# Performance work log

Hardware: AMD Instinct MI355X
Metric: run time of the kernel (lower is better)

Reference implementation:

```python
import jax, jax.numpy as jnp
import numpy as np

N_DRUG, N_DIS = 100_000, 50_000
E1, E2 = 500_000, 250_000
D, H = 128, 4
HD = D // H          # 32
EAD, CONT, CARD = 32, 4, 8


def _segment_softmax(logits, seg, num_segments):
    # logits: [E, H], seg: [E] -> softmax normalized per destination node (PyG softmax)
    m = jax.ops.segment_max(logits, seg, num_segments=num_segments)
    m = jnp.where(jnp.isfinite(m), m, 0.0)  # empty segments
    ex = jnp.exp(logits - m[seg])
    s = jax.ops.segment_sum(ex, seg, num_segments=num_segments)
    return ex / (s[seg] + 1e-16)


def _edge_conv(src_x, dst_x, si, di, Wsrc, bsrc, Wdst, bdst, attn, gate):
    num_dst = dst_x.shape[0]
    msg_src = src_x[si] @ Wsrc + bsrc            # [E, D]
    msg_dst = dst_x[di] @ Wdst + bdst            # [E, D]
    msg = msg_src + msg_dst
    if gate is not None:
        msg = msg * gate
    E = msg.shape[0]
    mh = msg.reshape(E, H, HD)
    sh = msg_src.reshape(E, H, HD)
    dh = msg_dst.reshape(E, H, HD)
    logits = (sh * dh).sum(-1) * (1.0 / np.sqrt(HD)) + (mh * attn[None]).sum(-1)  # [E, H]
    w = _segment_softmax(logits, di, num_dst)    # [E, H]; dropout p applied only in training
    out = (mh * w[..., None]).reshape(E, D)
    return jax.ops.segment_sum(out, di, num_segments=num_dst)  # [num_dst, D]


def setup_inputs() -> dict:
    key = jax.random.key(0)
    it = iter(jax.random.split(key, 32))
    def nrm(shape, s=0.05):
        return jax.random.normal(next(it), shape, jnp.float32) * s
    def ri(hi, shape):
        return jax.random.randint(next(it), shape, 0, hi, jnp.int32)
    z = lambda n: jnp.zeros((n,), jnp.float32)
    return {
        "x_drug": nrm((N_DRUG, D), 1.0),
        "x_dis": nrm((N_DIS, D), 1.0),
        "e1_cont": nrm((E1, CONT), 1.0),
        "W_src1": nrm((D, D)), "b_src1": z(D),
        "W_dst1": nrm((D, D)), "b_dst1": z(D),
        "attn1": nrm((H, HD)),
        "emb1": nrm((CARD, EAD)),
        "gW1": nrm((EAD + CONT, D)), "gb1": z(D),
        "gW2": nrm((D, D)), "gb2": z(D),
        "W_src2": nrm((D, D)), "b_src2": z(D),
        "W_dst2": nrm((D, D)), "b_dst2": z(D),
        "attn2": nrm((H, HD)),
        "Wo_drug": nrm((D, D)), "bo_drug": z(D),
        "Wo_dis": nrm((D, D)), "bo_dis": z(D),
        "e1_src": ri(N_DRUG, (E1,)), "e1_dst": ri(N_DRUG, (E1,)),
        "e2_src": ri(N_DRUG, (E2,)), "e2_dst": ri(N_DIS, (E2,)),
        "e1_cat": ri(CARD, (E1,)),
    }


def reference(x_drug, x_dis, e1_cont, W_src1, b_src1, W_dst1, b_dst1, attn1,
              emb1, gW1, gb1, gW2, gb2, W_src2, b_src2, W_dst2, b_dst2, attn2,
              Wo_drug, bo_drug, Wo_dis, bo_dis,
              e1_src, e1_dst, e2_src, e2_dst, e1_cat):
    # drug -> drug edges, spec mixed (1 categorical + 4 continuous): gated messages
    gate_feat = jnp.concatenate([emb1[e1_cat], e1_cont], axis=-1)  # [E1, EAD+CONT]
    gate = jax.nn.sigmoid(
        jax.nn.gelu(gate_feat @ gW1 + gb1, approximate=False) @ gW2 + gb2)  # [E1, D]
    aggr_drug = _edge_conv(x_drug, x_drug, e1_src, e1_dst,
                           W_src1, b_src1, W_dst1, b_dst1, attn1, gate)
    # drug -> disease edges, spec none: no gate
    aggr_dis = _edge_conv(x_drug, x_dis, e2_src, e2_dst,
                          W_src2, b_src2, W_dst2, b_dst2, attn2, None)
    # one message list per dst node type -> mean over a single element == identity
    out_drug = aggr_drug @ Wo_drug + bo_drug
    out_dis = aggr_dis @ Wo_dis + bo_dis
    return (out_drug, out_dis)
```

## Files before the change

kernel.cpp:

```cpp
#include <hip/hip_runtime.h>
#include <hip/hip_bf16.h>
#include <math.h>

#define ND 100000
#define NS 50000
#define NE1 500000
#define NE2 250000
#define DIM 128
#define NH 4
#define HDI 32
#define GRID_M 512
#define GRID_G 1024
#define GRID_E1 2048
#define GRID_E2 1024
#define NT1 (NE1 / 16)
#define NT2 (NE2 / 16)

typedef __hip_bfloat16 bf16;
typedef unsigned short u16;
typedef unsigned int u32;
typedef short sx8 __attribute__((ext_vector_type(8)));
typedef float fx4 __attribute__((ext_vector_type(4)));

__device__ __forceinline__ float ldf(const float* p, size_t i) { return p[i]; }
__device__ __forceinline__ float ldf(const bf16* p, size_t i) { return __bfloat162float(p[i]); }
__device__ __forceinline__ float b2f(bf16 v) { return __bfloat162float(v); }

__device__ __forceinline__ u16 f2bfu(float f) {
    __hip_bfloat16 h = __float2bfloat16(f);
    union { __hip_bfloat16 b; u16 u; } c; c.b = h; return c.u;
}
__device__ __forceinline__ float2 bfp(u32 u) {
    float2 r;
    r.x = __uint_as_float(u << 16);
    r.y = __uint_as_float(u & 0xffff0000u);
    return r;
}
__device__ __forceinline__ sx8 pack8(float4 v0, float4 v1) {
    sx8 r;
    r[0] = (short)f2bfu(v0.x); r[1] = (short)f2bfu(v0.y);
    r[2] = (short)f2bfu(v0.z); r[3] = (short)f2bfu(v0.w);
    r[4] = (short)f2bfu(v1.x); r[5] = (short)f2bfu(v1.y);
    r[6] = (short)f2bfu(v1.z); r[7] = (short)f2bfu(v1.w);
    return r;
}
__device__ __forceinline__ sx8 lda8(const bf16* p) { return *(const sx8*)p; }
__device__ __forceinline__ sx8 lda8(const float* p) {
    return pack8(*(const float4*)p, *(const float4*)(p + 4));
}
__device__ __forceinline__ float4 ld4(const float* p) { return *(const float4*)p; }
__device__ __forceinline__ float4 ld4(const bf16* p) {
    float2 a = bfp(*(const u32*)p);
    float2 b = bfp(*(const u32*)(p + 2));
    return make_float4(a.x, a.y, b.x, b.y);
}

__device__ __forceinline__ float gelu_fast(float x) {
    float u2 = x * fmaf(x * x, 0.0713550f, 1.5957691f);
    u2 = fminf(u2, 40.0f);
    float t = __expf(u2);
    return x * t * __builtin_amdgcn_rcpf(t + 1.0f);
}
__device__ __forceinline__ float sigmoid_fast(float x) {
    return __builtin_amdgcn_rcpf(1.0f + __expf(-x));
}
__device__ __forceinline__ float exp_fast(float x) { return __expf(x); }

__device__ __forceinline__ void slab_store(float* Gw, const fx4* acc, int er, int lg) {
#pragma unroll
    for (int f = 0; f < 8; ++f)
#pragma unroll
        for (int r = 0; r < 4; ++r) {
            int row = 4 * lg + r;
            int byo = row * 512 + (((16 * f + er) * 4) ^ ((row & 7) << 4));
            *(float*)((char*)Gw + byo) = acc[f][r];
        }
}
__device__ __forceinline__ void slab_flush_bf16(const float* Gw, int lane, bf16* Yrow) {
#pragma unroll
    for (int i = 0; i < 16; ++i) {
        float2 gv = *(const float2*)((const char*)Gw + i * 512 + ((lane * 8) ^ ((i & 7) << 4)));
        u32 pk = ((u32)f2bfu(gv.y) << 16) | (u32)f2bfu(gv.x);
        *(u32*)&Yrow[(size_t)i * DIM + 2 * lane] = pk;
    }
}
__device__ __forceinline__ void sty2(float* p, float2 v) { *(float2*)p = v; }
__device__ __forceinline__ void sty2(bf16* p, float2 v) {
    *(u32*)p = ((u32)f2bfu(v.y) << 16) | (u32)f2bfu(v.x);
}

__global__ void fill16_kernel(u16* p, u16 v, size_t n) {
    size_t i = (size_t)blockIdx.x * blockDim.x + threadIdx.x;
    if (i < n) p[i] = v;
}

__global__ __launch_bounds__(64) void detect_kernel(const u16* w, int* flag) {
    int lane = threadIdx.x;
    int mx = 0;
    for (int j = 0; j < 32; ++j) {
        int i = 2 * (lane + 64 * j);
        int e = (w[i] >> 7) & 0xFF;
        mx = mx > e ? mx : e;
    }
    for (int d = 32; d; d >>= 1) { int o = __shfl_xor(mx, d); mx = mx > o ? mx : o; }
    if (lane == 0) flag[0] = (mx >= 0x90) ? 1 : 0;
}

__global__ __launch_bounds__(256) void hist_kernel(const int* __restrict__ dst, int ne,
                                                   u32* __restrict__ cnt) {
    int stride = gridDim.x * blockDim.x;
    for (int i = blockIdx.x * blockDim.x + threadIdx.x; i < ne; i += stride)
        atomicAdd(&cnt[dst[i]], 1u);
}

__global__ __launch_bounds__(256) void scanA_kernel(const u32* __restrict__ cnt, int nb,
                                                    u32* __restrict__ chk) {
    __shared__ u32 ws[4];
    int b = blockIdx.x, t = threadIdx.x;
    int i0 = b * 1024 + t * 4;
    u32 s = 0;
#pragma unroll
    for (int j = 0; j < 4; ++j) { int i = i0 + j; if (i < nb) s += cnt[i]; }
#pragma unroll
    for (int d = 1; d < 64; d <<= 1) s += __shfl_xor(s, d);
    if ((t & 63) == 0) ws[t >> 6] = s;
    __syncthreads();
    if (t == 0) chk[b] = ws[0] + ws[1] + ws[2] + ws[3];
}

__global__ __launch_bounds__(256) void scanB_kernel(u32* __restrict__ chk, int nc) {
    __shared__ u32 sh[256];
    int t = threadIdx.x;
    u32 v = (t < nc) ? chk[t] : 0u;
    sh[t] = v;
    __syncthreads();
    for (int d = 1; d < 256; d <<= 1) {
        u32 x = (t >= d) ? sh[t - d] : 0u;
        __syncthreads();
        if (t >= d) sh[t] += x;
        __syncthreads();
    }
    if (t < nc) chk[t] = sh[t] - v;
}

__global__ __launch_bounds__(256) void scanC_kernel(const u32* __restrict__ cnt, int nb,
                                                    const u32* __restrict__ chk,
                                                    u32* __restrict__ offs) {
    __shared__ u32 wsum[4];
    int b = blockIdx.x, t = threadIdx.x, lane = t & 63, wv = t >> 6;
    int i0 = b * 1024 + t * 4;
    u32 c0 = (i0 + 0 < nb) ? cnt[i0 + 0] : 0u;
    u32 c1 = (i0 + 1 < nb) ? cnt[i0 + 1] : 0u;
    u32 c2 = (i0 + 2 < nb) ? cnt[i0 + 2] : 0u;
    u32 c3 = (i0 + 3 < nb) ? cnt[i0 + 3] : 0u;
    u32 tot = c0 + c1 + c2 + c3;
    u32 inc = tot;
#pragma unroll
    for (int d = 1; d < 64; d <<= 1) { u32 x = __shfl_up(inc, d); if (lane >= d) inc += x; }
    if (lane == 63) wsum[wv] = inc;
    __syncthreads();
    u32 base = chk[b] + (inc - tot);
    for (int k = 0; k < wv; ++k) base += wsum[k];
    if (i0 + 0 < nb) offs[i0 + 0] = base;
    if (i0 + 1 < nb) offs[i0 + 1] = base + c0;
    if (i0 + 2 < nb) offs[i0 + 2] = base + c0 + c1;
    if (i0 + 3 < nb) offs[i0 + 3] = base + c0 + c1 + c2;
}

__global__ __launch_bounds__(256) void scatter_kernel(const int* __restrict__ dst, int ne,
                                                      u32* __restrict__ offs,
                                                      u32* __restrict__ perm) {
    int stride = gridDim.x * blockDim.x;
    for (int i = blockIdx.x * blockDim.x + threadIdx.x; i < ne; i += stride) {
        u32 p = atomicAdd(&offs[dst[i]], 1u);
        perm[p] = (u32)i;
    }
}

template <typename T>
__device__ __forceinline__ void transp(const T* W, u16* Bt, int gtid, int gstride) {
    for (int i = gtid; i < DIM * DIM; i += gstride) {
        int n = i >> 7, k = i & 127;
        Bt[i] = f2bfu(ldf(W, (size_t)k * DIM + n));
    }
}

template <typename T>
__device__ __forceinline__ void prep_body(
    const T* emb, const T* gW1, const T* gb1, const T* gW2,
    const T* Ws1, const T* Wd1, const T* Ws2, const T* Wd2, const T* Wod, const T* Wos,
    u16* B1t, float* gb2f, const T* gb2,
    u16* Btg, u16* Bs1, u16* Bd1, u16* Bs2, u16* Bd2, u16* Bod, u16* Bos)
{
    int gtid = blockIdx.x * blockDim.x + threadIdx.x;
    int gstride = gridDim.x * blockDim.x;
    for (int i = gtid; i < DIM * 32; i += gstride) {
        int n = i >> 5, k = i & 31;
        float v = 0.0f;
        if (k < 8) {
            v = ldf(gb1, n);
            for (int q = 0; q < 32; ++q) v += ldf(emb, k * 32 + q) * ldf(gW1, (size_t)q * DIM + n);
        } else if (k < 12) {
            v = ldf(gW1, (size_t)(32 + (k - 8)) * DIM + n);
        }
        B1t[i] = f2bfu(v);
    }
    for (int i = gtid; i < DIM; i += gstride) gb2f[i] = ldf(gb2, i);
    transp(gW2, Btg, gtid, gstride);
    transp(Ws1, Bs1, gtid, gstride);
    transp(Wd1, Bd1, gtid, gstride);
    transp(Ws2, Bs2, gtid, gstride);
    transp(Wd2, Bd2, gtid, gstride);
    transp(Wod, Bod, gtid, gstride);
    transp(Wos, Bos, gtid, gstride);
}

__global__ __launch_bounds__(256) void prep_kernel(
    const int* __restrict__ flag,
    const void* emb, const void* gW1, const void* gb1, const void* gW2, const void* gb2,
    const void* Ws1, const void* Wd1, const void* Ws2, const void* Wd2,
    const void* Wod, const void* Wos,
    u16* __restrict__ B1t, float* __restrict__ gb2f,
    u16* __restrict__ Btg, u16* __restrict__ Bs1, u16* __restrict__ Bd1,
    u16* __restrict__ Bs2, u16* __restrict__ Bd2, u16* __restrict__ Bod,
    u16* __restrict__ Bos)
{
    if (flag[0])
        prep_body((const float*)emb, (const float*)gW1, (const float*)gb1, (const float*)gW2,
                  (const float*)Ws1, (const float*)Wd1, (const float*)Ws2, (const float*)Wd2,
                  (const float*)Wod, (const float*)Wos,
                  B1t, gb2f, (const float*)gb2, Btg, Bs1, Bd1, Bs2, Bd2, Bod, Bos);
    else
        prep_body((const bf16*)emb, (const bf16*)gW1, (const bf16*)gb1, (const bf16*)gW2,
                  (const bf16*)Ws1, (const bf16*)Wd1, (const bf16*)Ws2, (const bf16*)Wd2,
                  (const bf16*)Wod, (const bf16*)Wos,
                  B1t, gb2f, (const bf16*)gb2, Btg, Bs1, Bd1, Bs2, Bd2, Bod, Bos);
}

template <typename T>
__device__ __forceinline__ void proj2m_body(
    float* Gw, const T* X, const T* b1, const T* b2,
    const u16* Bt1, const u16* Bt2, bf16* Y1, bf16* Y2, int N)
{
    int tid = threadIdx.x, lane = tid & 63, er = lane & 15, lg = lane >> 4;
    float c1i[8], c2i[8];
#pragma unroll
    for (int f = 0; f < 8; ++f) {
        c1i[f] = ldf(b1, 16 * f + er);
        c2i[f] = ldf(b2, 16 * f + er);
    }
    const int NW = GRID_M * 4;
    int gwid = blockIdx.x * 4 + (tid >> 6);
    int tiles = N / 16;
    for (int t = gwid; t < tiles; t += NW) {
        const T* xr = X + (size_t)(t * 16 + er) * DIM;
        sx8 a[4];
#pragma unroll
        for (int ks = 0; ks < 4; ++ks) a[ks] = lda8(xr + ks * 32 + lg * 8);
        fx4 acc1[8], acc2[8];
#pragma unroll
        for (int f = 0; f < 8; ++f) {
            acc1[f][0] = c1i[f]; acc1[f][1] = c1i[f]; acc1[f][2] = c1i[f]; acc1[f][3] = c1i[f];
            acc2[f][0] = c2i[f]; acc2[f][1] = c2i[f]; acc2[f][2] = c2i[f]; acc2[f][3] = c2i[f];
        }
#pragma unroll
        for (int ks = 0; ks < 4; ++ks)
#pragma unroll
            for (int f = 0; f < 8; ++f) {
                sx8 bv1 = *(const sx8*)(Bt1 + (size_t)(16 * f + er) * DIM + ks * 32 + lg * 8);
                acc1[f] = __builtin_amdgcn_mfma_f32_16x16x32_bf16(a[ks], bv1, acc1[f], 0, 0, 0);
                sx8 bv2 = *(const sx8*)(Bt2 + (size_t)(16 * f + er) * DIM + ks * 32 + lg * 8);
                acc2[f] = __builtin_amdgcn_mfma_f32_16x16x32_bf16(a[ks], bv2, acc2[f], 0, 0, 0);
            }
        slab_store(Gw, acc1, er, lg);
        slab_flush_bf16(Gw, lane, Y1 + (size_t)t * 16 * DIM);
        slab_store(Gw, acc2, er, lg);
        slab_flush_bf16(Gw, lane, Y2 + (size_t)t * 16 * DIM);
    }
}

__global__ __launch_bounds__(256) void proj2m_kernel(
    const int* __restrict__ flag, const void* X, const void* b1, const void* b2,
    const u16* __restrict__ Bt1, const u16* __restrict__ Bt2,
    bf16* __restrict__ Y1, bf16* __restrict__ Y2, int N)
{
    __shared__ float Gt[4][16 * 128];
    float* Gw = Gt[threadIdx.x >> 6];
    if (flag[0]) proj2m_body(Gw, (const float*)X, (const float*)b1, (const float*)b2, Bt1, Bt2, Y1, Y2, N);
    else         proj2m_body(Gw, (const bf16*)X, (const bf16*)b1, (const bf16*)b2, Bt1, Bt2, Y1, Y2, N);
}

template <typename T>
__device__ __forceinline__ void proj1m_body(
    float* Gw, const T* X, const T* b, const u16* Bt, bf16* Y, int N)
{
    int tid = threadIdx.x, lane = tid & 63, er = lane & 15, lg = lane >> 4;
    float ci[8];
#pragma unroll
    for (int f = 0; f < 8; ++f) ci[f] = ldf(b, 16 * f + er);
    const int NW = GRID_M * 4;
    int gwid = blockIdx.x * 4 + (tid >> 6);
    int tiles = N / 16;
    for (int t = gwid; t < tiles; t += NW) {
        const T* xr = X + (size_t)(t * 16 + er) * DIM;
        sx8 a[4];
#pragma unroll
        for (int ks = 0; ks < 4; ++ks) a[ks] = lda8(xr + ks * 32 + lg * 8);
        fx4 acc[8];
#pragma unroll
        for (int f = 0; f < 8; ++f) {
            acc[f][0] = ci[f]; acc[f][1] = ci[f]; acc[f][2] = ci[f]; acc[f][3] = ci[f];
        }
#pragma unroll
        for (int ks = 0; ks < 4; ++ks)
#pragma unroll
            for (int f = 0; f < 8; ++f) {
                sx8 bv = *(const sx8*)(Bt + (size_t)(16 * f + er) * DIM + ks * 32 + lg * 8);
                acc[f] = __builtin_amdgcn_mfma_f32_16x16x32_bf16(a[ks], bv, acc[f], 0, 0, 0);
            }
        slab_store(Gw, acc, er, lg);
        slab_flush_bf16(Gw, lane, Y + (size_t)t * 16 * DIM);
    }
}

__global__ __launch_bounds__(256) void proj1m_kernel(
    const int* __restrict__ flag, const void* X, const void* b,
    const u16* __restrict__ Bt, bf16* __restrict__ Y, int N)
{
    __shared__ float Gt[4][16 * 128];
    float* Gw = Gt[threadIdx.x >> 6];
    if (flag[0]) proj1m_body(Gw, (const float*)X, (const float*)b, Bt, Y, N);
    else         proj1m_body(Gw, (const bf16*)X, (const bf16*)b, Bt, Y, N);
}

template <typename T>
__device__ __forceinline__ void projoutm_body(
    float* Gw, const float* A, const float* s, const T* b,
    const u16* Bt, T* out, int N)
{
    int tid = threadIdx.x, lane = tid & 63, er = lane & 15, lg = lane >> 4;
    float ci[8];
#pragma unroll
    for (int f = 0; f < 8; ++f) ci[f] = ldf(b, 16 * f + er);
    const int NW = GRID_M * 4;
    int gwid = blockIdx.x * 4 + (tid >> 6);
    int tiles = N / 16;
    for (int t = gwid; t < tiles; t += NW) {
        const float* ar = A + (size_t)(t * 16 + er) * DIM;
        const float* sr = s + (size_t)(t * 16 + er) * NH;
        sx8 a[4];
#pragma unroll
        for (int ks = 0; ks < 4; ++ks) {
            float inv = 1.0f / (sr[ks] + 1e-16f);
            float4 v0 = *(const float4*)(ar + ks * 32 + lg * 8);
            float4 v1 = *(const float4*)(ar + ks * 32 + lg * 8 + 4);
            v0.x *= inv; v0.y *= inv; v0.z *= inv; v0.w *= inv;
            v1.x *= inv; v1.y *= inv; v1.z *= inv; v1.w *= inv;
            a[ks] = pack8(v0, v1);
        }
        fx4 acc[8];
#pragma unroll
        for (int f = 0; f < 8; ++f) {
            acc[f][0] = ci[f]; acc[f][1] = ci[f]; acc[f][2] = ci[f]; acc[f][3] = ci[f];
        }
#pragma unroll
        for (int ks = 0; ks < 4; ++ks)
#pragma unroll
            for (int f = 0; f < 8; ++f) {
                sx8 bv = *(const sx8*)(Bt + (size_t)(16 * f + er) * DIM + ks * 32 + lg * 8);
                acc[f] = __builtin_amdgcn_mfma_f32_16x16x32_bf16(a[ks], bv, acc[f], 0, 0, 0);
            }
        slab_store(Gw, acc, er, lg);
#pragma unroll
        for (int i = 0; i < 16; ++i) {
            float2 gv = *(const float2*)((const char*)Gw + i * 512 + ((lane * 8) ^ ((i & 7) << 4)));
            sty2(out + (size_t)(t * 16 + i) * DIM + 2 * lane, gv);
        }
    }
}

__global__ __launch_bounds__(256) void projoutm_kernel(
    const int* __restrict__ flag, const float* __restrict__ A, const float* __restrict__ s,
    const void* b, const u16* __restrict__ Bt, void* out, size_t off, int N)
{
    __shared__ float Gt[4][16 * 128];
    float* Gw = Gt[threadIdx.x >> 6];
    if (flag[0]) projoutm_body(Gw, A, s, (const float*)b, Bt, (float*)out + off, N);
    else         projoutm_body(Gw, A, s, (const bf16*)b, Bt, (bf16*)out + off, N);
}

template <typename T>
__device__ __forceinline__ void gateall_body(
    float* Gw, const int* cat, const T* econt,
    const float* gb2f, const u16* B1t, const u16* Btg,
    const u32* perm, u32* gates, int c0, int c1)
{
    int tid = threadIdx.x;
    int lane = tid & 63;
    int er = lane & 15, lg = lane >> 4;

    float cinit[8];
#pragma unroll
    for (int f = 0; f < 8; ++f) cinit[f] = gb2f[16 * f + er];

    const int NW = GRID_G * 4;
    int span = c1 - c0;
    int w = blockIdx.x * 4 + (tid >> 6);
    int tpw = (span + NW - 1) / NW;
    int t0 = c0 + w * tpw, t1 = t0 + tpw;
    if (t1 > c1) t1 = c1;

    const fx4 zf = {0.f, 0.f, 0.f, 0.f};

    int c = 0;
    float4 fv = make_float4(0.f, 0.f, 0.f, 0.f);
    if (t0 < t1) {
        int e = (int)perm[t0 * 16 + er];
        c = cat[e];
        fv = ld4(econt + (size_t)e * 4);
    }

    for (int t = t0; t < t1; ++t) {
        int tn = t + 1;
        int e_n = (tn < t1) ? (int)perm[tn * 16 + er] : 0;
        int c_n = cat[e_n];
        float4 fv_n = ld4(econt + (size_t)e_n * 4);

        sx8 a1;
#pragma unroll
        for (int j = 0; j < 8; ++j) a1[j] = 0;
        if (lg == 0) {
#pragma unroll
            for (int j = 0; j < 8; ++j) a1[j] = (c == j) ? (short)0x3F80 : (short)0;
        } else if (lg == 1) {
            a1[0] = (short)f2bfu(fv.x); a1[1] = (short)f2bfu(fv.y);
            a1[2] = (short)f2bfu(fv.z); a1[3] = (short)f2bfu(fv.w);
        }

        fx4 p1[8];
#pragma unroll
        for (int f = 0; f < 8; ++f) {
            sx8 b1 = *(const sx8*)(B1t + (size_t)(16 * f + er) * 32 + lg * 8);
            p1[f] = __builtin_amdgcn_mfma_f32_16x16x32_bf16(a1, b1, zf, 0, 0, 0);
        }

#pragma unroll
        for (int f = 0; f < 8; ++f)
#pragma unroll
            for (int r = 0; r < 4; ++r) {
                int row = 4 * lg + r;
                float hg = gelu_fast(p1[f][r]);
                int byo = row * 512 + (((16 * f + er) * 4) ^ ((row & 7) << 4));
                *(float*)((char*)Gw + byo) = hg;
            }

        sx8 a2[4];
#pragma unroll
        for (int ks = 0; ks < 4; ++ks) {
            int base = ks * 128 + lg * 32;
            float4 v0 = *(const float4*)((const char*)Gw + er * 512 + ((base)      ^ ((er & 7) << 4)));
            float4 v1 = *(const float4*)((const char*)Gw + er * 512 + ((base + 16) ^ ((er & 7) << 4)));
            a2[ks] = pack8(v0, v1);
        }

        fx4 acc[8];
#pragma unroll
        for (int f = 0; f < 8; ++f) {
            acc[f][0] = cinit[f]; acc[f][1] = cinit[f];
            acc[f][2] = cinit[f]; acc[f][3] = cinit[f];
        }
#pragma unroll
        for (int ks = 0; ks < 4; ++ks) {
#pragma unroll
            for (int f = 0; f < 8; ++f) {
                sx8 b = *(const sx8*)(Btg + (size_t)(16 * f + er) * DIM + ks * 32 + lg * 8);
                acc[f] = __builtin_amdgcn_mfma_f32_16x16x32_bf16(a2[ks], b, acc[f], 0, 0, 0);
            }
        }

#pragma unroll
        for (int f = 0; f < 8; ++f)
#pragma unroll
            for (int r = 0; r < 4; ++r) {
                int row = 4 * lg + r;
                float g = sigmoid_fast(acc[f][r]);
                int byo = row * 512 + (((16 * f + er) * 4) ^ ((row & 7) << 4));
                *(float*)((char*)Gw + byo) = g;
            }

#pragma unroll
        for (int i = 0; i < 16; ++i) {
            float2 gv = *(const float2*)((const char*)Gw + i * 512 + ((lane * 8) ^ ((i & 7) << 4)));
            u32 pk = ((u32)f2bfu(gv.y) << 16) | (u32)f2bfu(gv.x);
            gates[((size_t)(t - c0) * 16 + i) * 64 + lane] = pk;
        }

        c = c_n; fv = fv_n;
    }
}

__global__ __launch_bounds__(256) void gateall_kernel(
    const int* __restrict__ flag, const int* __restrict__ cat, const void* econt,
    const float* __restrict__ gb2f, const u16* __restrict__ B1t,
    const u16* __restrict__ Btg,
    const u32* __restrict__ perm, u32* __restrict__ gates, int c0, int c1)
{
    __shared__ float Gt[4][16 * 128];
    float* Gw = Gt[threadIdx.x >> 6];
    if (flag[0]) gateall_body(Gw, cat, (const float*)econt, gb2f, B1t, Btg, perm, gates, c0, c1);
    else         gateall_body(Gw, cat, (const bf16*)econt, gb2f, B1t, Btg, perm, gates, c0, c1);
}

template <typename T>
__device__ __forceinline__ void edge1e_body(
    const bf16* Xs, const bf16* Xd,
    const int* src, const int* dst,
    const T* attn, const u32* perm, const u32* gates, int c0, int c1,
    float* s_out, float* aggr)
{
    int tid = threadIdx.x;
    int lane = tid & 63;
    int d0 = 2 * lane, h = lane >> 4, k0 = d0 & 31;
    float av0 = ldf(attn, h * HDI + k0), av1 = ldf(attn, h * HDI + k0 + 1);
    const float rs = 0.17677669529663688110f;

    const int NW = GRID_E1 * 4;
    int span = c1 - c0;
    int w = blockIdx.x * 4 + (tid >> 6);
    int cpw = (span + NW - 1) / NW;
    int t0 = c0 + w * cpw, t1 = t0 + cpw;
    if (t1 > c1) t1 = c1;

    int cur_di = -1;
    float acc0 = 0.f, acc1 = 0.f, ssum = 0.f;

    u32 sv = 0, dv = 0;
    if (t0 < t1 && lane < 16) {
        u32 pe = perm[t0 * 16 + lane];
        sv = (u32)src[(int)pe];
        dv = (u32)dst[(int)pe];
    }

    for (int t = t0; t < t1; ++t) {
        u32 sv_n = 0, dv_n = 0;
        int tn = t + 1;
        if (tn < t1 && lane < 16) {
            u32 pe_n = perm[tn * 16 + lane];
            sv_n = (u32)src[(int)pe_n];
            dv_n = (u32)dst[(int)pe_n];
        }

        u32 xsp[16], xdp[16], gp[16];
#pragma unroll
        for (int i = 0; i < 16; ++i) {
            int si = (int)__builtin_amdgcn_readlane(sv, i);
            int di = (int)__builtin_amdgcn_readlane(dv, i);
            xsp[i] = *(const u32*)&Xs[(size_t)si * DIM + d0];
            xdp[i] = *(const u32*)&Xd[(size_t)di * DIM + d0];
            gp[i]  = gates[((size_t)(t - c0) * 16 + i) * 64 + lane];
        }
#pragma unroll
        for (int i = 0; i < 16; ++i) {
            int di = (int)__builtin_amdgcn_readlane(dv, i);
            float2 sxy = bfp(xsp[i]);
            float2 dxy = bfp(xdp[i]);
            float2 gxy = bfp(gp[i]);
            if (di != cur_di) {
                if (cur_di >= 0) {
                    float* ap = &aggr[(size_t)cur_di * DIM + d0];
                    atomicAdd(ap, acc0);
                    atomicAdd(ap + 1, acc1);
                    if ((lane & 15) == 0)
                        atomicAdd(&s_out[(size_t)cur_di * NH + h], ssum);
                }
                cur_di = di; acc0 = 0.f; acc1 = 0.f; ssum = 0.f;
            }
            float m0 = (sxy.x + dxy.x) * gxy.x;
            float m1 = (sxy.y + dxy.y) * gxy.y;
            float p = (sxy.x * dxy.x + sxy.y * dxy.y) * rs + m0 * av0 + m1 * av1;
            p += __shfl_xor(p, 8);
            p += __shfl_xor(p, 4);
            p += __shfl_xor(p, 2);
            p += __shfl_xor(p, 1);
            float ev = exp_fast(fminf(p, 80.0f));
            acc0 = fmaf(ev, m0, acc0);
            acc1 = fmaf(ev, m1, acc1);
            ssum += ev;
        }

        sv = sv_n; dv = dv_n;
    }
    if (cur_di >= 0) {
        float* ap = &aggr[(size_t)cur_di * DIM + d0];
        atomicAdd(ap, acc0);
        atomicAdd(ap + 1, acc1);
        if ((lane & 15) == 0)
            atomicAdd(&s_out[(size_t)cur_di * NH + h], ssum);
    }
}

__global__ __launch_bounds__(256) void edge1e_kernel(
    const int* __restrict__ flag,
    const bf16* __restrict__ Xs, const bf16* __restrict__ Xd,
    const int* __restrict__ src, const int* __restrict__ dst,
    const void* attn, const u32* __restrict__ perm, const u32* __restrict__ gates,
    int c0, int c1, float* __restrict__ s_out, float* __restrict__ aggr)
{
    if (flag[0]) edge1e_body(Xs, Xd, src, dst, (const float*)attn, perm, gates, c0, c1, s_out, aggr);
    else         edge1e_body(Xs, Xd, src, dst, (const bf16*)attn, perm, gates, c0, c1, s_out, aggr);
}

template <typename T>
__device__ __forceinline__ void edge2e_body(
    const bf16* Xs, const bf16* Xd,
    const int* src, const int* dst,
    const T* attn, const u32* perm, float* s_out, float* aggr)
{
    int tid = threadIdx.x;
    int lane = tid & 63;
    int d0 = 2 * lane, h = lane >> 4, k0 = d0 & 31;
    float av0 = ldf(attn, h * HDI + k0), av1 = ldf(attn, h * HDI + k0 + 1);
    const float rs = 0.17677669529663688110f;

    const int NW = GRID_E2 * 4;
    int w = blockIdx.x * 4 + (tid >> 6);
    int cpw = (NT2 + NW - 1) / NW;
    int t0 = w * cpw, t1 = t0 + cpw;
    if (t1 > NT2) t1 = NT2;

    int cur_di = -1;
    float acc0 = 0.f, acc1 = 0.f, ssum = 0.f;

    u32 sv = 0, dv = 0;
    if (t0 < t1 && lane < 16) {
        u32 pe = perm[t0 * 16 + lane];
        sv = (u32)src[(int)pe];
        dv = (u32)dst[(int)pe];
    }

    for (int t = t0; t < t1; ++t) {
        u32 sv_n = 0, dv_n = 0;
        int tn = t + 1;
        if (tn < t1 && lane < 16) {
            u32 pe_n = perm[tn * 16 + lane];
            sv_n = (u32)src[(int)pe_n];
            dv_n = (u32)dst[(int)pe_n];
        }

        u32 xsp[16], xdp[16];
#pragma unroll
        for (int i = 0; i < 16; ++i) {
            int si = (int)__builtin_amdgcn_readlane(sv, i);
            int di = (int)__builtin_amdgcn_readlane(dv, i);
            xsp[i] = *(const u32*)&Xs[(size_t)si * DIM + d0];
            xdp[i] = *(const u32*)&Xd[(size_t)di * DIM + d0];
        }
#pragma unroll
        for (int i = 0; i < 16; ++i) {
            int di = (int)__builtin_amdgcn_readlane(dv, i);
            float2 sxy = bfp(xsp[i]);
            float2 dxy = bfp(xdp[i]);
            if (di != cur_di) {
                if (cur_di >= 0) {
                    float* ap = &aggr[(size_t)cur_di * DIM + d0];
                    atomicAdd(ap, acc0);
                    atomicAdd(ap + 1, acc1);
                    if ((lane & 15) == 0)
                        atomicAdd(&s_out[(size_t)cur_di * NH + h], ssum);
                }
                cur_di = di; acc0 = 0.f; acc1 = 0.f; ssum = 0.f;
            }
            float m0 = sxy.x + dxy.x;
            float m1 = sxy.y + dxy.y;
            float p = (sxy.x * dxy.x + sxy.y * dxy.y) * rs + m0 * av0 + m1 * av1;
            p += __shfl_xor(p, 8);
            p += __shfl_xor(p, 4);
            p += __shfl_xor(p, 2);
            p += __shfl_xor(p, 1);
            float ev = exp_fast(fminf(p, 80.0f));
            acc0 = fmaf(ev, m0, acc0);
            acc1 = fmaf(ev, m1, acc1);
            ssum += ev;
        }

        sv = sv_n; dv = dv_n;
    }
    if (cur_di >= 0) {
        float* ap = &aggr[(size_t)cur_di * DIM + d0];
        atomicAdd(ap, acc0);
        atomicAdd(ap + 1, acc1);
        if ((lane & 15) == 0)
            atomicAdd(&s_out[(size_t)cur_di * NH + h], ssum);
    }
}

__global__ __launch_bounds__(256) void edge2e_kernel(
    const int* __restrict__ flag,
    const bf16* __restrict__ Xs, const bf16* __restrict__ Xd,
    const int* __restrict__ src, const int* __restrict__ dst,
    const void* attn, const u32* __restrict__ perm,
    float* __restrict__ s_out, float* __restrict__ aggr)
{
    if (flag[0]) edge2e_body(Xs, Xd, src, dst, (const float*)attn, perm, s_out, aggr);
    else         edge2e_body(Xs, Xd, src, dst, (const bf16*)attn, perm, s_out, aggr);
}

extern "C" void kernel_launch(void* const* d_in, const int* in_sizes, int n_in,
                              void* d_out, int out_size, void* d_ws, size_t ws_size,
                              hipStream_t stream)
{
    const void* x_drug  = d_in[0];
    const void* x_dis   = d_in[1];
    const void* e1_cont = d_in[2];
    const void* W_src1  = d_in[3];
    const void* b_src1  = d_in[4];
    const void* W_dst1  = d_in[5];
    const void* b_dst1  = d_in[6];
    const void* attn1   = d_in[7];
    const void* emb1    = d_in[8];
    const void* gW1     = d_in[9];
    const void* gb1     = d_in[10];
    const void* gW2     = d_in[11];
    const void* gb2     = d_in[12];
    const void* W_src2  = d_in[13];
    const void* b_src2  = d_in[14];
    const void* W_dst2  = d_in[15];
    const void* b_dst2  = d_in[16];
    const void* attn2   = d_in[17];
    const void* Wo_drug = d_in[18];
    const void* bo_drug = d_in[19];
    const void* Wo_dis  = d_in[20];
    const void* bo_dis  = d_in[21];
    const int* e1_src = (const int*)d_in[22];
    const int* e1_dst = (const int*)d_in[23];
    const int* e2_src = (const int*)d_in[24];
    const int* e2_dst = (const int*)d_in[25];
    const int* e1_cat = (const int*)d_in[26];

    bool sizes_ok = (n_in == 27)
        && in_sizes[0] == ND * DIM && in_sizes[1] == NS * DIM
        && in_sizes[2] == NE1 * 4
        && in_sizes[3] == DIM * DIM && in_sizes[4] == DIM
        && in_sizes[5] == DIM * DIM && in_sizes[6] == DIM
        && in_sizes[7] == NH * HDI && in_sizes[8] == 8 * 32
        && in_sizes[9] == 36 * DIM && in_sizes[10] == DIM
        && in_sizes[11] == DIM * DIM && in_sizes[12] == DIM
        && in_sizes[13] == DIM * DIM && in_sizes[17] == NH * HDI
        && in_sizes[18] == DIM * DIM && in_sizes[20] == DIM * DIM
        && in_sizes[22] == NE1 && in_sizes[23] == NE1
        && in_sizes[24] == NE2 && in_sizes[25] == NE2 && in_sizes[26] == NE1;
    if (!sizes_ok) {
        size_t n = (size_t)out_size;
        fill16_kernel<<<(int)((n + 255) / 256), 256, 0, stream>>>((u16*)d_out, 0x429A, n);
        return;
    }

    size_t off_B1   = 64;
    size_t off_g2   = off_B1 + (size_t)DIM * 32 * 2;
    size_t off_Bt   = off_g2 + DIM * 4;
    size_t off_Bs1  = off_Bt  + (size_t)DIM * DIM * 2;
    size_t off_Bd1  = off_Bs1 + (size_t)DIM * DIM * 2;
    size_t off_Bs2  = off_Bd1 + (size_t)DIM * DIM * 2;
    size_t off_Bd2  = off_Bs2 + (size_t)DIM * DIM * 2;
    size_t off_Bod  = off_Bd2 + (size_t)DIM * DIM * 2;
    size_t off_Bos  = off_Bod + (size_t)DIM * DIM * 2;
    size_t off_Xs   = off_Bos + (size_t)DIM * DIM * 2;
    size_t off_Xd   = off_Xs + (size_t)ND * DIM * 2;
    size_t off_sb   = off_Xd + (size_t)ND * DIM * 2;
    size_t off_aggr = off_sb + (size_t)ND * NH * 4;
    size_t off_cnt  = off_aggr + (size_t)ND * DIM * 4;
    size_t off_offs = off_cnt + (size_t)(ND + 16) * 4;
    size_t off_chk  = off_offs + (size_t)(ND + 16) * 4;
    size_t off_p1   = off_chk + 512;
    size_t off_p2   = off_p1 + (size_t)NE1 * 4;
    size_t off_gate = (off_p2 + (size_t)NE2 * 4 + 255) & ~(size_t)255;
    if (ws_size < off_gate) {
        size_t n = (size_t)out_size;
        fill16_kernel<<<(int)((n + 255) / 256), 256, 0, stream>>>((u16*)d_out, 0x42F6, n);
        return;
    }

    int cpp = 8192;
    while (cpp >= 1024 && off_gate + (size_t)cpp * 16 * 256 > ws_size) cpp >>= 1;
    if (off_gate + (size_t)cpp * 16 * 256 > ws_size) {
        size_t n = (size_t)out_size;
        fill16_kernel<<<(int)((n + 255) / 256), 256, 0, stream>>>((u16*)d_out, 0x42F6, n);
        return;
    }
    int nparts = (NT1 + cpp - 1) / cpp;

    char* w = (char*)d_ws;
    int*   flag = (int*)w;
    u16*   B1t  = (u16*)(w + off_B1);
    float* gb2p = (float*)(w + off_g2);
    u16*   Btg  = (u16*)(w + off_Bt);
    u16*   Bs1  = (u16*)(w + off_Bs1);
    u16*   Bd1  = (u16*)(w + off_Bd1);
    u16*   Bs2  = (u16*)(w + off_Bs2);
    u16*   Bd2  = (u16*)(w + off_Bd2);
    u16*   Bod  = (u16*)(w + off_Bod);
    u16*   Bos  = (u16*)(w + off_Bos);
    bf16*  Xs   = (bf16*)(w + off_Xs);
    bf16*  Xd   = (bf16*)(w + off_Xd);
    float* sb   = (float*)(w + off_sb);
    float* aggr = (float*)(w + off_aggr);
    u32*   cnt  = (u32*)(w + off_cnt);
    u32*   offs = (u32*)(w + off_offs);
    u32*   chk  = (u32*)(w + off_chk);
    u32*   perm1 = (u32*)(w + off_p1);
    u32*   perm2 = (u32*)(w + off_p2);
    u32*   gates = (u32*)(w + off_gate);

    detect_kernel<<<1, 64, 0, stream>>>((const u16*)W_src1, flag);
    prep_kernel<<<64, 256, 0, stream>>>(flag, emb1, gW1, gb1, gW2, gb2,
                                        W_src1, W_dst1, W_src2, W_dst2, Wo_drug, Wo_dis,
                                        B1t, gb2p, Btg, Bs1, Bd1, Bs2, Bd2, Bod, Bos);

    hipMemsetAsync(cnt, 0, (size_t)(ND + 16) * 4, stream);
    hist_kernel<<<1024, 256, 0, stream>>>(e1_dst, NE1, cnt);
    scanA_kernel<<<98, 256, 0, stream>>>(cnt, ND, chk);
    scanB_kernel<<<1, 256, 0, stream>>>(chk, 98);
    scanC_kernel<<<98, 256, 0, stream>>>(cnt, ND, chk, offs);
    scatter_kernel<<<1024, 256, 0, stream>>>(e1_dst, NE1, offs, perm1);

    hipMemsetAsync(sb, 0, (size_t)ND * NH * 4, stream);
    hipMemsetAsync(aggr, 0, (size_t)ND * DIM * 4, stream);
    proj2m_kernel<<<GRID_M, 256, 0, stream>>>(flag, x_drug, b_src1, b_dst1, Bs1, Bd1, Xs, Xd, ND);
    for (int part = 0; part < nparts; ++part) {
        int c0 = part * cpp, c1 = c0 + cpp;
        if (c1 > NT1) c1 = NT1;
        if (c0 >= c1) break;
        gateall_kernel<<<GRID_G, 256, 0, stream>>>(flag, e1_cat, e1_cont,
                                                   gb2p, B1t, Btg, perm1, gates, c0, c1);
        edge1e_kernel<<<GRID_E1, 256, 0, stream>>>(flag, Xs, Xd, e1_src, e1_dst,
                                                   attn1, perm1, gates, c0, c1, sb, aggr);
    }
    projoutm_kernel<<<GRID_M, 256, 0, stream>>>(flag, aggr, sb, bo_drug, Bod, d_out, 0, ND);

    hipMemsetAsync(cnt, 0, (size_t)(NS + 16) * 4, stream);
    hist_kernel<<<1024, 256, 0, stream>>>(e2_dst, NE2, cnt);
    scanA_kernel<<<49, 256, 0, stream>>>(cnt, NS, chk);
    scanB_kernel<<<1, 256, 0, stream>>>(chk, 49);
    scanC_kernel<<<49, 256, 0, stream>>>(cnt, NS, chk, offs);
    scatter_kernel<<<1024, 256, 0, stream>>>(e2_dst, NE2, offs, perm2);

    hipMemsetAsync(sb, 0, (size_t)NS * NH * 4, stream);
    hipMemsetAsync(aggr, 0, (size_t)NS * DIM * 4, stream);
    proj1m_kernel<<<GRID_M, 256, 0, stream>>>(flag, x_drug, b_src2, Bs2, Xs, ND);
    proj1m_kernel<<<GRID_M, 256, 0, stream>>>(flag, x_dis, b_dst2, Bd2, Xd, NS);
    edge2e_kernel<<<GRID_E2, 256, 0, stream>>>(flag, Xs, Xd, e2_src, e2_dst, attn2, perm2, sb, aggr);
    projoutm_kernel<<<GRID_M, 256, 0, stream>>>(flag, aggr, sb, bo_dis, Bos, d_out, (size_t)ND * DIM, NS);
}
```

Baseline: 788.2 us.

## Software-pipeline edge gathers one tile ahead and enlarge grids and gate chunk

The edge aggregation kernels now issue the gathers for the next 16-edge tile of source/destination features (and gates) before computing the current tile, and prefetch indices two tiles ahead. This double-buffering is meant to hide gather latency behind the softmax-weighted accumulation. Grid sizes for the gate and edge2 kernels are doubled, and the gate partition size is raised to cover all edge-1 tiles when the workspace allows, which reduces the number of partitions. The cost is higher register pressure from the double buffers, which may lower occupancy.

```diff
diff --git a/kernel.cpp b/kernel.cpp
--- a/kernel.cpp
+++ b/kernel.cpp
@@ -10,9 +10,9 @@
 #define NH 4
 #define HDI 32
 #define GRID_M 512
-#define GRID_G 1024
+#define GRID_G 2048
 #define GRID_E1 2048
-#define GRID_E2 1024
+#define GRID_E2 2048
 #define NT1 (NE1 / 16)
 #define NT2 (NE2 / 16)
 
@@ -530,41 +530,58 @@
     int cpw = (span + NW - 1) / NW;
     int t0 = c0 + w * cpw, t1 = t0 + cpw;
     if (t1 > c1) t1 = c1;
+    if (t0 >= t1) return;
 
     int cur_di = -1;
     float acc0 = 0.f, acc1 = 0.f, ssum = 0.f;
 
-    u32 sv = 0, dv = 0;
-    if (t0 < t1 && lane < 16) {
+    u32 svA = 0, dvA = 0;
+    if (lane < 16) {
         u32 pe = perm[t0 * 16 + lane];
-        sv = (u32)src[(int)pe];
-        dv = (u32)dst[(int)pe];
+        svA = (u32)src[(int)pe];
+        dvA = (u32)dst[(int)pe];
+    }
+    u32 xspA[16], xdpA[16], gpA[16];
+#pragma unroll
+    for (int i = 0; i < 16; ++i) {
+        int si = (int)__builtin_amdgcn_readlane(svA, i);
+        int di = (int)__builtin_amdgcn_readlane(dvA, i);
+        xspA[i] = *(const u32*)&Xs[(size_t)si * DIM + d0];
+        xdpA[i] = *(const u32*)&Xd[(size_t)di * DIM + d0];
+        gpA[i]  = gates[((size_t)(t0 - c0) * 16 + i) * 64 + lane];
+    }
+    u32 svB = 0, dvB = 0;
+    if (t0 + 1 < t1 && lane < 16) {
+        u32 pe = perm[(t0 + 1) * 16 + lane];
+        svB = (u32)src[(int)pe];
+        dvB = (u32)dst[(int)pe];
     }
 
     for (int t = t0; t < t1; ++t) {
-        u32 sv_n = 0, dv_n = 0;
-        int tn = t + 1;
-        if (tn < t1 && lane < 16) {
-            u32 pe_n = perm[tn * 16 + lane];
-            sv_n = (u32)src[(int)pe_n];
-            dv_n = (u32)dst[(int)pe_n];
-        }
-
-        u32 xsp[16], xdp[16], gp[16];
+        u32 xspB[16], xdpB[16], gpB[16];
+        if (t + 1 < t1) {
+#pragma unroll
+            for (int i = 0; i < 16; ++i) {
+                int si = (int)__builtin_amdgcn_readlane(svB, i);
+                int di = (int)__builtin_amdgcn_readlane(dvB, i);
+                xspB[i] = *(const u32*)&Xs[(size_t)si * DIM + d0];
+                xdpB[i] = *(const u32*)&Xd[(size_t)di * DIM + d0];
+                gpB[i]  = gates[((size_t)(t + 1 - c0) * 16 + i) * 64 + lane];
+            }
+        }
+        u32 svC = 0, dvC = 0;
+        if (t + 2 < t1 && lane < 16) {
+            u32 pe = perm[(t + 2) * 16 + lane];
+            svC = (u32)src[(int)pe];
+            dvC = (u32)dst[(int)pe];
+        }
+
 #pragma unroll
         for (int i = 0; i < 16; ++i) {
-            int si = (int)__builtin_amdgcn_readlane(sv, i);
-            int di = (int)__builtin_amdgcn_readlane(dv, i);
-            xsp[i] = *(const u32*)&Xs[(size_t)si * DIM + d0];
-            xdp[i] = *(const u32*)&Xd[(size_t)di * DIM + d0];
-            gp[i]  = gates[((size_t)(t - c0) * 16 + i) * 64 + lane];
-        }
-#pragma unroll
-        for (int i = 0; i < 16; ++i) {
-            int di = (int)__builtin_amdgcn_readlane(dv, i);
-            float2 sxy = bfp(xsp[i]);
-            float2 dxy = bfp(xdp[i]);
-            float2 gxy = bfp(gp[i]);
+            int di = (int)__builtin_amdgcn_readlane(dvA, i);
+            float2 sxy = bfp(xspA[i]);
+            float2 dxy = bfp(xdpA[i]);
+            float2 gxy = bfp(gpA[i]);
             if (di != cur_di) {
                 if (cur_di >= 0) {
                     float* ap = &aggr[(size_t)cur_di * DIM + d0];
@@ -588,7 +605,11 @@
             ssum += ev;
         }
 
-        sv = sv_n; dv = dv_n;
+        svA = svB; dvA = dvB; svB = svC; dvB = dvC;
+#pragma unroll
+        for (int i = 0; i < 16; ++i) {
+            xspA[i] = xspB[i]; xdpA[i] = xdpB[i]; gpA[i] = gpB[i];
+        }
     }
     if (cur_di >= 0) {
         float* ap = &aggr[(size_t)cur_di * DIM + d0];
@@ -627,39 +648,55 @@
     int cpw = (NT2 + NW - 1) / NW;
     int t0 = w * cpw, t1 = t0 + cpw;
     if (t1 > NT2) t1 = NT2;
+    if (t0 >= t1) return;
 
     int cur_di = -1;
     float acc0 = 0.f, acc1 = 0.f, ssum = 0.f;
 
-    u32 sv = 0, dv = 0;
-    if (t0 < t1 && lane < 16) {
+    u32 svA = 0, dvA = 0;
+    if (lane < 16) {
         u32 pe = perm[t0 * 16 + lane];
-        sv = (u32)src[(int)pe];
-        dv = (u32)dst[(int)pe];
+        svA = (u32)src[(int)pe];
+        dvA = (u32)dst[(int)pe];
+    }
+    u32 xspA[16], xdpA[16];
+#pragma unroll
+    for (int i = 0; i < 16; ++i) {
+        int si = (int)__builtin_amdgcn_readlane(svA, i);
+        int di = (int)__builtin_amdgcn_readlane(dvA, i);
+        xspA[i] = *(const u32*)&Xs[(size_t)si * DIM + d0];
+        xdpA[i] = *(const u32*)&Xd[(size_t)di * DIM + d0];
+    }
+    u32 svB = 0, dvB = 0;
+    if (t0 + 1 < t1 && lane < 16) {
+        u32 pe = perm[(t0 + 1) * 16 + lane];
+        svB = (u32)src[(int)pe];
+        dvB = (u32)dst[(int)pe];
     }
 
     for (int t = t0; t < t1; ++t) {
-        u32 sv_n = 0, dv_n = 0;
-        int tn = t + 1;
-        if (tn < t1 && lane < 16) {
-            u32 pe_n = perm[tn * 16 + lane];
-            sv_n = (u32)src[(int)pe_n];
-            dv_n = (u32)dst[(int)pe_n];
-        }
-
-        u32 xsp[16], xdp[16];
+        u32 xspB[16], xdpB[16];
+        if (t + 1 < t1) {
+#pragma unroll
+            for (int i = 0; i < 16; ++i) {
+                int si = (int)__builtin_amdgcn_readlane(svB, i);
+                int di = (int)__builtin_amdgcn_readlane(dvB, i);
+                xspB[i] = *(const u32*)&Xs[(size_t)si * DIM + d0];
+                xdpB[i] = *(const u32*)&Xd[(size_t)di * DIM + d0];
+            }
+        }
+        u32 svC = 0, dvC = 0;
+        if (t + 2 < t1 && lane < 16) {
+            u32 pe = perm[(t + 2) * 16 + lane];
+            svC = (u32)src[(int)pe];
+            dvC = (u32)dst[(int)pe];
+        }
+
 #pragma unroll
         for (int i = 0; i < 16; ++i) {
-            int si = (int)__builtin_amdgcn_readlane(sv, i);
-            int di = (int)__builtin_amdgcn_readlane(dv, i);
-            xsp[i] = *(const u32*)&Xs[(size_t)si * DIM + d0];
-            xdp[i] = *(const u32*)&Xd[(size_t)di * DIM + d0];
-        }
-#pragma unroll
-        for (int i = 0; i < 16; ++i) {
-            int di = (int)__builtin_amdgcn_readlane(dv, i);
-            float2 sxy = bfp(xsp[i]);
-            float2 dxy = bfp(xdp[i]);
+            int di = (int)__builtin_amdgcn_readlane(dvA, i);
+            float2 sxy = bfp(xspA[i]);
+            float2 dxy = bfp(xdpA[i]);
             if (di != cur_di) {
                 if (cur_di >= 0) {
                     float* ap = &aggr[(size_t)cur_di * DIM + d0];
@@ -683,7 +720,9 @@
             ssum += ev;
         }
 
-        sv = sv_n; dv = dv_n;
+        svA = svB; dvA = dvB; svB = svC; dvB = dvC;
+#pragma unroll
+        for (int i = 0; i < 16; ++i) { xspA[i] = xspB[i]; xdpA[i] = xdpB[i]; }
     }
     if (cur_di >= 0) {
         float* ap = &aggr[(size_t)cur_di * DIM + d0];
@@ -780,7 +819,7 @@
         return;
     }
 
-    int cpp = 8192;
+    int cpp = NT1;
     while (cpp >= 1024 && off_gate + (size_t)cpp * 16 * 256 > ws_size) cpp >>= 1;
     if (off_gate + (size_t)cpp * 16 * 256 > ws_size) {
         size_t n = (size_t)out_size;
```

After: 733.5 us. 6.9% less time.
